# Performance work log

Hardware: AMD Instinct MI355X
Metric: run time of the kernel (lower is better)

The kernel has to match this reference:

```python
import jax, jax.numpy as jnp
import numpy as np

T, D = 2048, 2048
H, H_KV, DH = 32, 8, 64
I = 5632
EPS = 1e-5


def setup_inputs() -> dict:
    key = jax.random.key(0)
    ks = jax.random.split(key, 9)
    s = 0.02
    return {
        "x": jax.random.normal(ks[0], (T, D), dtype=jnp.float32),
        "ln1_w": jnp.ones((D,), dtype=jnp.float32),
        "ln2_w": jnp.ones((D,), dtype=jnp.float32),
        "wq": jax.random.normal(ks[1], (D, H * DH), dtype=jnp.float32) * s,
        "wk": jax.random.normal(ks[2], (D, H_KV * DH), dtype=jnp.float32) * s,
        "wv": jax.random.normal(ks[3], (D, H_KV * DH), dtype=jnp.float32) * s,
        "wo": jax.random.normal(ks[4], (H * DH, D), dtype=jnp.float32) * s,
        "w1": jax.random.normal(ks[5], (D, 2 * I), dtype=jnp.float32) * s,
        "w2": jax.random.normal(ks[6], (I, D), dtype=jnp.float32) * s,
    }


def _rmsnorm(x, w):
    var = jnp.mean(x * x, axis=-1, keepdims=True)
    return x * jax.lax.rsqrt(var + EPS) * w


def reference(x, ln1_w, ln2_w, wq, wk, wv, wo, w1, w2):
    t, d = x.shape
    h = _rmsnorm(x, ln1_w)
    # projections -> (heads, T, head_dim)
    q = (h @ wq).reshape(t, H, DH).transpose(1, 0, 2)
    k = (h @ wk).reshape(t, H_KV, DH).transpose(1, 0, 2)
    v = (h @ wv).reshape(t, H_KV, DH).transpose(1, 0, 2)
    # GQA: query head hq uses kv head hq * H_KV // H == hq // (H // H_KV)
    rep = H // H_KV
    k = jnp.repeat(k, rep, axis=0)  # (H, T, DH)
    v = jnp.repeat(v, rep, axis=0)
    scale = 1.0 / np.sqrt(DH)
    scores = jnp.einsum('htd,hsd->hts', q, k) * scale  # (H, T, T)
    causal = jnp.tril(jnp.ones((t, t), dtype=bool))
    neg = jnp.asarray(jnp.finfo(scores.dtype).min, scores.dtype)
    scores = jnp.where(causal[None, :, :], scores, neg)
    weights = jax.nn.softmax(scores, axis=-1)
    attn = jnp.einsum('hts,hsd->htd', weights, v)  # (H, T, DH)
    attn = attn.transpose(1, 0, 2).reshape(t, H * DH)
    x = x + attn @ wo
    h2 = _rmsnorm(x, ln2_w)
    fc1 = h2 @ w1  # (T, 2I)
    gate, val = fc1[:, :I], fc1[:, I:]
    sw = jax.nn.silu(gate) * val
    return x + sw @ w2
```

## Files before the change

kernel.cpp:

```cpp
#include <hip/hip_runtime.h>
#include <hip/hip_bf16.h>
#include <cstdint>
#include <cstddef>

#define TT 2048
#define DD 2048
#define NHQ 32
#define NHKV 8
#define DHD 64
#define II 5632

typedef short short8 __attribute__((ext_vector_type(8)));
typedef __bf16 bf16x8 __attribute__((ext_vector_type(8)));
typedef float f32x4 __attribute__((ext_vector_type(4)));

__device__ __forceinline__ float b2f(unsigned short u) {
  union { float f; unsigned int i; } v; v.i = ((unsigned int)u) << 16; return v.f;
}
__device__ __forceinline__ unsigned short f2b(float f) {
  union { float f; unsigned int i; } v; v.f = f;
  unsigned int r = v.i + 0x7FFFu + ((v.i >> 16) & 1u);
  return (unsigned short)(r >> 16);
}

__global__ void transpose_f32_bf16(const float* __restrict__ src,
                                   unsigned short* __restrict__ dst,
                                   int K, int N) {
  __shared__ float tile[32][33];
  const int bn = blockIdx.x * 32;
  const int bk = blockIdx.y * 32;
  const int tx = threadIdx.x, ty = threadIdx.y;
#pragma unroll
  for (int i = 0; i < 32; i += 8)
    tile[ty + i][tx] = src[(size_t)(bk + ty + i) * N + bn + tx];
  __syncthreads();
#pragma unroll
  for (int i = 0; i < 32; i += 8)
    dst[(size_t)(bn + ty + i) * K + bk + tx] = f2b(tile[tx][ty + i]);
}

__global__ void rmsnorm_kernel(const float* __restrict__ x,
                               const float* __restrict__ w,
                               unsigned short* __restrict__ out) {
  const int row = blockIdx.x;
  const float* xr = x + (size_t)row * DD;
  const int t = threadIdx.x;
  float4 v0 = ((const float4*)xr)[t];
  float4 v1 = ((const float4*)xr)[t + 256];
  float ss = v0.x * v0.x + v0.y * v0.y + v0.z * v0.z + v0.w * v0.w +
             v1.x * v1.x + v1.y * v1.y + v1.z * v1.z + v1.w * v1.w;
#pragma unroll
  for (int off = 32; off >= 1; off >>= 1) ss += __shfl_xor(ss, off);
  __shared__ float sred[4];
  if ((t & 63) == 0) sred[t >> 6] = ss;
  __syncthreads();
  float tot = sred[0] + sred[1] + sred[2] + sred[3];
  float rs = rsqrtf(tot * (1.0f / DD) + 1e-5f);
  float4 w0 = ((const float4*)w)[t];
  float4 w1v = ((const float4*)w)[t + 256];
  unsigned short* orow = out + (size_t)row * DD;
  ushort4 o0, o1;
  o0.x = f2b(v0.x * rs * w0.x); o0.y = f2b(v0.y * rs * w0.y);
  o0.z = f2b(v0.z * rs * w0.z); o0.w = f2b(v0.w * rs * w0.w);
  o1.x = f2b(v1.x * rs * w1v.x); o1.y = f2b(v1.y * rs * w1v.y);
  o1.z = f2b(v1.z * rs * w1v.z); o1.w = f2b(v1.w * rs * w1v.w);
  ((ushort4*)orow)[t] = o0;
  ((ushort4*)orow)[t + 256] = o1;
}

template <int EPI>
__launch_bounds__(256, 2)
__global__ void gemm_bt(const unsigned short* __restrict__ A, int lda,
                        const unsigned short* __restrict__ Bt, int ldb,
                        int K,
                        const float* __restrict__ resid,
                        void* __restrict__ Cout, int ldc) {
  constexpr int BKP = 40;
  __shared__ __align__(16) unsigned short As[128 * BKP];
  __shared__ __align__(16) unsigned short Bs[128 * BKP];
  const int bm = blockIdx.y * 128;
  const int bn = blockIdx.x * 128;
  const int tid = threadIdx.x;
  const int lane = tid & 63;
  const int L = lane & 15, G = lane >> 4;
  const int w = tid >> 6;
  const int wr = (w >> 1) * 64, wc = (w & 1) * 64;

  const f32x4 zero = {0.f, 0.f, 0.f, 0.f};
  f32x4 acc[4][4];
#pragma unroll
  for (int m = 0; m < 4; ++m)
#pragma unroll
    for (int n = 0; n < 4; ++n) acc[m][n] = zero;

  const int sr = tid >> 2;
  const int sc = (tid & 3) * 8;
  const unsigned short* Ab = A + (size_t)(bm + sr) * lda + sc;
  const unsigned short* Bb = Bt + (size_t)(bn + sr) * ldb + sc;

  const int nk = K >> 5;
  for (int kt = 0; kt < nk; ++kt) {
    const int ko = kt * 32;
    short8 ra0 = *(const short8*)(Ab + ko);
    short8 ra1 = *(const short8*)(Ab + (size_t)64 * lda + ko);
    short8 rb0 = *(const short8*)(Bb + ko);
    short8 rb1 = *(const short8*)(Bb + (size_t)64 * ldb + ko);
    __syncthreads();
    *(short8*)&As[sr * BKP + sc] = ra0;
    *(short8*)&As[(sr + 64) * BKP + sc] = ra1;
    *(short8*)&Bs[sr * BKP + sc] = rb0;
    *(short8*)&Bs[(sr + 64) * BKP + sc] = rb1;
    __syncthreads();
    bf16x8 af[4], bf[4];
#pragma unroll
    for (int m = 0; m < 4; ++m)
      af[m] = *reinterpret_cast<const bf16x8*>(&As[(wr + m * 16 + L) * BKP + G * 8]);
#pragma unroll
    for (int n = 0; n < 4; ++n)
      bf[n] = *reinterpret_cast<const bf16x8*>(&Bs[(wc + n * 16 + L) * BKP + G * 8]);
#pragma unroll
    for (int m = 0; m < 4; ++m)
#pragma unroll
      for (int n = 0; n < 4; ++n)
        acc[m][n] = __builtin_amdgcn_mfma_f32_16x16x32_bf16(af[m], bf[n], acc[m][n], 0, 0, 0);
  }

#pragma unroll
  for (int m = 0; m < 4; ++m)
#pragma unroll
    for (int n = 0; n < 4; ++n)
#pragma unroll
      for (int i = 0; i < 4; ++i) {
        const int r = bm + wr + m * 16 + G * 4 + i;
        const int c = bn + wc + n * 16 + L;
        const float val = acc[m][n][i];
        if constexpr (EPI == 0) {
          ((unsigned short*)Cout)[(size_t)r * ldc + c] = f2b(val);
        } else {
          ((float*)Cout)[(size_t)r * ldc + c] = val + resid[(size_t)r * ldc + c];
        }
      }
}

__launch_bounds__(256, 2)
__global__ void attn_kernel(const unsigned short* __restrict__ qkv,
                            unsigned short* __restrict__ out) {
  const int hq = blockIdx.x;
  const int qb = blockIdx.y;
  const int hkv = hq >> 2;
  const int tid = threadIdx.x, lane = tid & 63, w = tid >> 6;
  const int L = lane & 15, G = lane >> 4;

  __shared__ __align__(16) unsigned short Ks[64 * 72];
  __shared__ __align__(16) unsigned short Vt[64 * 72];
  __shared__ __align__(16) unsigned short Ps[4][16 * 72];

  const int qrow = qb * 64 + w * 16;
  bf16x8 qf[2];
#pragma unroll
  for (int d0 = 0; d0 < 2; ++d0)
    qf[d0] = *reinterpret_cast<const bf16x8*>(
        qkv + (size_t)(qrow + L) * 3072 + hq * 64 + d0 * 32 + G * 8);

  const f32x4 zero = {0.f, 0.f, 0.f, 0.f};
  f32x4 o[4];
#pragma unroll
  for (int n = 0; n < 4; ++n) o[n] = zero;
  float mrow[4], lrow[4];
#pragma unroll
  for (int i = 0; i < 4; ++i) { mrow[i] = -1e30f; lrow[i] = 0.f; }

  const int ntile = qb + 1;
  for (int t = 0; t < ntile; ++t) {
    const int s0 = t * 64;
    __syncthreads();
#pragma unroll
    for (int i2 = 0; i2 < 2; ++i2) {
      const int c = i2 * 256 + tid;
      const int r = c >> 3, col = (c & 7) * 8;
      bf16x8 k8 = *reinterpret_cast<const bf16x8*>(
          qkv + (size_t)(s0 + r) * 3072 + 2048 + hkv * 64 + col);
      *reinterpret_cast<bf16x8*>(&Ks[r * 72 + col]) = k8;
      short8 v8 = *reinterpret_cast<const short8*>(
          qkv + (size_t)(s0 + r) * 3072 + 2560 + hkv * 64 + col);
#pragma unroll
      for (int j = 0; j < 8; ++j)
        Vt[(col + j) * 72 + r] = (unsigned short)v8[j];
    }
    __syncthreads();

    f32x4 sacc[4];
#pragma unroll
    for (int nt = 0; nt < 4; ++nt) {
      sacc[nt] = zero;
#pragma unroll
      for (int d0 = 0; d0 < 2; ++d0) {
        bf16x8 kf = *reinterpret_cast<const bf16x8*>(
            &Ks[(nt * 16 + L) * 72 + d0 * 32 + G * 8]);
        sacc[nt] = __builtin_amdgcn_mfma_f32_16x16x32_bf16(qf[d0], kf, sacc[nt], 0, 0, 0);
      }
    }

    float pt[4][4];
#pragma unroll
    for (int i = 0; i < 4; ++i) {
      const int q = qrow + G * 4 + i;
      float mx = mrow[i];
#pragma unroll
      for (int nt = 0; nt < 4; ++nt) {
        float sv = sacc[nt][i] * 0.125f;
        const int s = s0 + nt * 16 + L;
        sv = (s <= q) ? sv : -1e30f;
        pt[i][nt] = sv;
        mx = fmaxf(mx, sv);
      }
#pragma unroll
      for (int off = 1; off < 16; off <<= 1) mx = fmaxf(mx, __shfl_xor(mx, off));
      const float scale_o = __expf(mrow[i] - mx);
      float rsum = 0.f;
#pragma unroll
      for (int nt = 0; nt < 4; ++nt) {
        const float p = __expf(pt[i][nt] - mx);
        pt[i][nt] = p;
        rsum += p;
      }
#pragma unroll
      for (int off = 1; off < 16; off <<= 1) rsum += __shfl_xor(rsum, off);
      mrow[i] = mx;
      lrow[i] = lrow[i] * scale_o + rsum;
#pragma unroll
      for (int nt = 0; nt < 4; ++nt) o[nt][i] *= scale_o;
    }

#pragma unroll
    for (int i = 0; i < 4; ++i)
#pragma unroll
      for (int nt = 0; nt < 4; ++nt)
        Ps[w][(G * 4 + i) * 72 + nt * 16 + L] = f2b(pt[i][nt]);
#pragma unroll
    for (int kc = 0; kc < 2; ++kc) {
      bf16x8 pf = *reinterpret_cast<const bf16x8*>(&Ps[w][L * 72 + kc * 32 + G * 8]);
#pragma unroll
      for (int nt = 0; nt < 4; ++nt) {
        bf16x8 vf = *reinterpret_cast<const bf16x8*>(
            &Vt[(nt * 16 + L) * 72 + kc * 32 + G * 8]);
        o[nt] = __builtin_amdgcn_mfma_f32_16x16x32_bf16(pf, vf, o[nt], 0, 0, 0);
      }
    }
  }

#pragma unroll
  for (int nt = 0; nt < 4; ++nt)
#pragma unroll
    for (int i = 0; i < 4; ++i) {
      const float val = o[nt][i] / lrow[i];
      out[(size_t)(qrow + G * 4 + i) * 2048 + hq * 64 + nt * 16 + L] = f2b(val);
    }
}

__global__ void swiglu_kernel(unsigned short* __restrict__ fc1) {
  const size_t total = (size_t)TT * (II / 8);
  const size_t idx = (size_t)blockIdx.x * blockDim.x + threadIdx.x;
  if (idx >= total) return;
  const int m = (int)(idx / (II / 8));
  const int jc = (int)(idx % (II / 8));
  unsigned short* g = fc1 + (size_t)m * (2 * II) + jc * 8;
  short8 gv = *(const short8*)g;
  short8 vv = *(const short8*)(g + II);
  short8 ov;
#pragma unroll
  for (int j = 0; j < 8; ++j) {
    const float gf = b2f((unsigned short)gv[j]);
    const float vf = b2f((unsigned short)vv[j]);
    const float s = gf / (1.f + __expf(-gf));
    ov[j] = (short)f2b(s * vf);
  }
  *(short8*)g = ov;
}

extern "C" void kernel_launch(void* const* d_in, const int* in_sizes, int n_in,
                              void* d_out, int out_size, void* d_ws, size_t ws_size,
                              hipStream_t stream) {
  const float* x    = (const float*)d_in[0];
  const float* ln1w = (const float*)d_in[1];
  const float* ln2w = (const float*)d_in[2];
  const float* wq   = (const float*)d_in[3];
  const float* wk   = (const float*)d_in[4];
  const float* wv   = (const float*)d_in[5];
  const float* wo   = (const float*)d_in[6];
  const float* w1   = (const float*)d_in[7];
  const float* w2   = (const float*)d_in[8];
  float* outp = (float*)d_out;

  char* ws = (char*)d_ws;
  size_t off = 0;
  auto alloc = [&](size_t bytes) {
    char* p = ws + off;
    off += (bytes + 255) & ~(size_t)255;
    return p;
  };
  unsigned short* wqkvT = (unsigned short*)alloc((size_t)3072 * 2048 * 2);
  unsigned short* woT   = (unsigned short*)alloc((size_t)2048 * 2048 * 2);
  unsigned short* w1T   = (unsigned short*)alloc((size_t)11264 * 2048 * 2);
  unsigned short* w2T   = (unsigned short*)alloc((size_t)2048 * 5632 * 2);
  unsigned short* h     = (unsigned short*)alloc((size_t)2048 * 2048 * 2);
  unsigned short* qkv   = (unsigned short*)alloc((size_t)2048 * 3072 * 2);
  unsigned short* attnb = (unsigned short*)alloc((size_t)2048 * 2048 * 2);
  float*          x2    = (float*)alloc((size_t)2048 * 2048 * 4);
  unsigned short* h2    = (unsigned short*)alloc((size_t)2048 * 2048 * 2);
  unsigned short* fc1   = (unsigned short*)alloc((size_t)2048 * 11264 * 2);
  (void)ws_size; (void)in_sizes; (void)n_in; (void)out_size;

  dim3 tb(32, 8);
  transpose_f32_bf16<<<dim3(2048 / 32, 2048 / 32), tb, 0, stream>>>(wq, wqkvT, 2048, 2048);
  transpose_f32_bf16<<<dim3(512 / 32, 2048 / 32), tb, 0, stream>>>(wk, wqkvT + (size_t)2048 * 2048, 2048, 512);
  transpose_f32_bf16<<<dim3(512 / 32, 2048 / 32), tb, 0, stream>>>(wv, wqkvT + (size_t)2560 * 2048, 2048, 512);
  transpose_f32_bf16<<<dim3(2048 / 32, 2048 / 32), tb, 0, stream>>>(wo, woT, 2048, 2048);
  transpose_f32_bf16<<<dim3(11264 / 32, 2048 / 32), tb, 0, stream>>>(w1, w1T, 2048, 11264);
  transpose_f32_bf16<<<dim3(2048 / 32, 5632 / 32), tb, 0, stream>>>(w2, w2T, 5632, 2048);

  rmsnorm_kernel<<<2048, 256, 0, stream>>>(x, ln1w, h);

  gemm_bt<0><<<dim3(3072 / 128, 2048 / 128), 256, 0, stream>>>(
      h, 2048, wqkvT, 2048, 2048, nullptr, qkv, 3072);

  attn_kernel<<<dim3(NHQ, TT / 64), 256, 0, stream>>>(qkv, attnb);

  gemm_bt<1><<<dim3(2048 / 128, 2048 / 128), 256, 0, stream>>>(
      attnb, 2048, woT, 2048, 2048, x, x2, 2048);

  rmsnorm_kernel<<<2048, 256, 0, stream>>>(x2, ln2w, h2);

  gemm_bt<0><<<dim3(11264 / 128, 2048 / 128), 256, 0, stream>>>(
      h2, 2048, w1T, 2048, 2048, nullptr, fc1, 11264);

  swiglu_kernel<<<5632, 256, 0, stream>>>(fc1);

  gemm_bt<1><<<dim3(2048 / 128, 2048 / 128), 256, 0, stream>>>(
      fc1, 11264, w2T, 5632, 5632, x2, outp, 2048);
}
```

Baseline: 719.7 us.

## Load GEMM tiles directly into LDS and swizzle attention P/V shared buffers

The GEMM now fills its A/B tiles with global_load_lds (direct global-to-LDS loads) instead of staging through registers. It drops the padded row stride and the launch-bounds hint. In the attention kernel, the transposed V tile and the per-warp P tile get an XOR swizzle on their shared-memory indices to cut bank conflicts on the transposed writes and fragment reads. The unpadded GEMM LDS layout may add bank conflicts on fragment reads, and without the launch bounds the register allocation and occupancy may change.

Result: faster. 679.6 us (-5.6%).

```diff
diff --git a/kernel.cpp b/kernel.cpp
--- a/kernel.cpp
+++ b/kernel.cpp
@@ -21,6 +21,13 @@
   union { float f; unsigned int i; } v; v.f = f;
   unsigned int r = v.i + 0x7FFFu + ((v.i >> 16) & 1u);
   return (unsigned short)(r >> 16);
+}
+
+__device__ __forceinline__ void gload16(const unsigned short* g, unsigned short* l) {
+  __builtin_amdgcn_global_load_lds(
+      (const __attribute__((address_space(1))) void*)g,
+      (__attribute__((address_space(3))) void*)(unsigned int)(uintptr_t)l,
+      16, 0, 0);
 }
 
 __global__ void transpose_f32_bf16(const float* __restrict__ src,
@@ -69,15 +76,13 @@
 }
 
 template <int EPI>
-__launch_bounds__(256, 2)
 __global__ void gemm_bt(const unsigned short* __restrict__ A, int lda,
                         const unsigned short* __restrict__ Bt, int ldb,
                         int K,
                         const float* __restrict__ resid,
                         void* __restrict__ Cout, int ldc) {
-  constexpr int BKP = 40;
-  __shared__ __align__(16) unsigned short As[128 * BKP];
-  __shared__ __align__(16) unsigned short Bs[128 * BKP];
+  __shared__ __align__(16) unsigned short As[128 * 32];
+  __shared__ __align__(16) unsigned short Bs[128 * 32];
   const int bm = blockIdx.y * 128;
   const int bn = blockIdx.x * 128;
   const int tid = threadIdx.x;
@@ -93,36 +98,36 @@
 #pragma unroll
     for (int n = 0; n < 4; ++n) acc[m][n] = zero;
 
-  const int sr = tid >> 2;
-  const int sc = (tid & 3) * 8;
-  const unsigned short* Ab = A + (size_t)(bm + sr) * lda + sc;
-  const unsigned short* Bb = Bt + (size_t)(bn + sr) * ldb + sc;
+  const int srow = w * 32 + (lane >> 2);
+  const int scol = (lane & 3) * 8;
+  const unsigned short* gA = A + (size_t)(bm + srow) * lda + scol;
+  const unsigned short* gB = Bt + (size_t)(bn + srow) * ldb + scol;
+  unsigned short* lA0 = &As[w * 1024];
+  unsigned short* lA1 = &As[w * 1024 + 512];
+  unsigned short* lB0 = &Bs[w * 1024];
+  unsigned short* lB1 = &Bs[w * 1024 + 512];
 
   const int nk = K >> 5;
   for (int kt = 0; kt < nk; ++kt) {
     const int ko = kt * 32;
-    short8 ra0 = *(const short8*)(Ab + ko);
-    short8 ra1 = *(const short8*)(Ab + (size_t)64 * lda + ko);
-    short8 rb0 = *(const short8*)(Bb + ko);
-    short8 rb1 = *(const short8*)(Bb + (size_t)64 * ldb + ko);
     __syncthreads();
-    *(short8*)&As[sr * BKP + sc] = ra0;
-    *(short8*)&As[(sr + 64) * BKP + sc] = ra1;
-    *(short8*)&Bs[sr * BKP + sc] = rb0;
-    *(short8*)&Bs[(sr + 64) * BKP + sc] = rb1;
+    gload16(gA + ko, lA0);
+    gload16(gA + (size_t)16 * lda + ko, lA1);
+    gload16(gB + ko, lB0);
+    gload16(gB + (size_t)16 * ldb + ko, lB1);
     __syncthreads();
-    bf16x8 af[4], bf[4];
+    bf16x8 af[4], bfr[4];
 #pragma unroll
     for (int m = 0; m < 4; ++m)
-      af[m] = *reinterpret_cast<const bf16x8*>(&As[(wr + m * 16 + L) * BKP + G * 8]);
+      af[m] = *reinterpret_cast<const bf16x8*>(&As[(wr + m * 16 + L) * 32 + G * 8]);
 #pragma unroll
     for (int n = 0; n < 4; ++n)
-      bf[n] = *reinterpret_cast<const bf16x8*>(&Bs[(wc + n * 16 + L) * BKP + G * 8]);
+      bfr[n] = *reinterpret_cast<const bf16x8*>(&Bs[(wc + n * 16 + L) * 32 + G * 8]);
 #pragma unroll
     for (int m = 0; m < 4; ++m)
 #pragma unroll
       for (int n = 0; n < 4; ++n)
-        acc[m][n] = __builtin_amdgcn_mfma_f32_16x16x32_bf16(af[m], bf[n], acc[m][n], 0, 0, 0);
+        acc[m][n] = __builtin_amdgcn_mfma_f32_16x16x32_bf16(af[m], bfr[n], acc[m][n], 0, 0, 0);
   }
 
 #pragma unroll
@@ -184,8 +189,10 @@
       short8 v8 = *reinterpret_cast<const short8*>(
           qkv + (size_t)(s0 + r) * 3072 + 2560 + hkv * 64 + col);
 #pragma unroll
-      for (int j = 0; j < 8; ++j)
-        Vt[(col + j) * 72 + r] = (unsigned short)v8[j];
+      for (int j = 0; j < 8; ++j) {
+        const int d = col + j;
+        Vt[d * 72 + (r ^ (((d >> 3) & 7) << 3))] = (unsigned short)v8[j];
+      }
     }
     __syncthreads();
 
@@ -233,17 +240,21 @@
     }
 
 #pragma unroll
-    for (int i = 0; i < 4; ++i)
+    for (int i = 0; i < 4; ++i) {
+      const int prow = G * 4 + i;
 #pragma unroll
       for (int nt = 0; nt < 4; ++nt)
-        Ps[w][(G * 4 + i) * 72 + nt * 16 + L] = f2b(pt[i][nt]);
+        Ps[w][prow * 72 + ((nt * 16 + L) ^ ((prow & 7) << 3))] = f2b(pt[i][nt]);
+    }
 #pragma unroll
     for (int kc = 0; kc < 2; ++kc) {
-      bf16x8 pf = *reinterpret_cast<const bf16x8*>(&Ps[w][L * 72 + kc * 32 + G * 8]);
+      bf16x8 pf = *reinterpret_cast<const bf16x8*>(
+          &Ps[w][L * 72 + ((kc * 32 + G * 8) ^ ((L & 7) << 3))]);
 #pragma unroll
       for (int nt = 0; nt < 4; ++nt) {
+        const int vrow = nt * 16 + L;
         bf16x8 vf = *reinterpret_cast<const bf16x8*>(
-            &Vt[(nt * 16 + L) * 72 + kc * 32 + G * 8]);
+            &Vt[vrow * 72 + ((kc * 32 + G * 8) ^ (((vrow >> 3) & 7) << 3))]);
         o[nt] = __builtin_amdgcn_mfma_f32_16x16x32_bf16(pf, vf, o[nt], 0, 0, 0);
       }
     }
```
